# Optimization experiments

Hardware: AMD Instinct MI355X
Metric: run time of the kernel (lower is better)

Reference implementation:

```python
import jax, jax.numpy as jnp
import numpy as np
import math

HIDDEN = 1024

def setup_inputs() -> dict:
    key = jax.random.key(0)
    k1, k2, k3, k4, k5 = jax.random.split(key, 5)
    s = 1.0 / math.sqrt(HIDDEN)
    return {
        "x": jax.random.normal(k1, (4, 2048, HIDDEN), dtype=jnp.float32),
        "W_qkv": jax.random.uniform(k2, (HIDDEN, 3 * HIDDEN), jnp.float32, -s, s),
        "b_qkv": jax.random.uniform(k3, (3 * HIDDEN,), jnp.float32, -s, s),
        "W_out": jax.random.uniform(k4, (HIDDEN, HIDDEN), jnp.float32, -s, s),
        "b_out": jax.random.uniform(k5, (HIDDEN,), jnp.float32, -s, s),
    }

def reference(x, W_qkv, b_qkv, W_out, b_out):
    # fused QKV projection: [b, s, 3h]
    qkv = jnp.einsum("bsh,hd->bsd", x, W_qkv) + b_qkv
    q, k, v = jnp.split(qkv, 3, axis=-1)
    scale = 1.0 / math.sqrt(x.shape[-1])
    scores = jnp.einsum("bqh,bkh->bqk", q, k) * scale  # [b, s, s]
    attn = jax.nn.softmax(scores, axis=-1)
    out = jnp.einsum("bqk,bkh->bqh", attn, v)
    return jnp.einsum("bsh,hd->bsd", out, W_out) + b_out
```

## Files before the change

### kernel.cpp

```cpp
#include <hip/hip_runtime.h>
#include <cstdint>
#include <cstddef>


typedef __bf16 bf16;
typedef __bf16 bf16x8 __attribute__((ext_vector_type(8)));
typedef __bf16 bf16x4 __attribute__((ext_vector_type(4)));
typedef float  f32x4  __attribute__((ext_vector_type(4)));

#define THREADS 512
#define UNIT 8192

__device__ __forceinline__ void gload_lds16(const bf16* g, bf16* l) {
  __builtin_amdgcn_global_load_lds(
      (const __attribute__((address_space(1))) unsigned int*)g,
      (__attribute__((address_space(3))) unsigned int*)l, 16, 0, 0);
}

__device__ __forceinline__ void stage_unit(const bf16* g0, long ld, bf16* ldsu, int tid) {
  const int wv = tid >> 6;
  #pragma unroll
  for (int j = 0; j < 2; ++j) {
    const int c = j * 512 + tid;
    const int r = c >> 3;
    const int sg = (c & 7) ^ (r & 7);
    const int cb = j * 512 + (wv << 6);
    gload_lds16(g0 + (long)r * ld + sg * 8, ldsu + (size_t)cb * 8);
  }
}

__device__ __forceinline__ bf16x8 rd_frag(const bf16* unitb, int r, int s) {
  return *(const bf16x8*)(unitb + (size_t)r * 64 + (size_t)((s ^ (r & 7)) * 8));
}

#define GATE(N)  asm volatile("s_waitcnt vmcnt(" #N ")" ::: "memory")
#define LGKM0()  asm volatile("s_waitcnt lgkmcnt(0)" ::: "memory")
#define SBAR()   __builtin_amdgcn_s_barrier()
#define SCHED0() __builtin_amdgcn_sched_barrier(0)

#define BM2 256
#define BN2 128
#define BK2 64
#define BUFELS (3*UNIT)

template <int MODE>
__device__ __forceinline__ void gemm2_body(
    const bf16* __restrict__ A, long sAz, int lda,
    const bf16* __restrict__ B, long sBz, int ldb, int K,
    bf16* __restrict__ p0, long sCz, bf16* __restrict__ p1, bf16* __restrict__ p2,
    float* __restrict__ fout, const float* __restrict__ bias, float scale) {
  __shared__ bf16 lds[3 * BUFELS];
  const int tid = threadIdx.x;
  const int wv = tid >> 6, ln = tid & 63;
  const int wr = wv >> 1, wc = wv & 1;
  const int lr = ln & 15, lh = ln >> 4;
  const int m0 = blockIdx.x * BM2, n0 = blockIdx.y * BN2;
  const int z = blockIdx.z;
  A += (long)z * sAz;
  B += (long)z * sBz;
  const bf16* Ag = A + (long)m0 * lda;
  const bf16* Bg = B + (long)n0 * ldb;
  const int NT = K / BK2;

  #pragma unroll
  for (int t = 0; t < 2; ++t) {
    bf16* bb = lds + t * BUFELS;
    stage_unit(Ag + t * BK2, lda, bb, tid);
    stage_unit(Ag + (long)128 * lda + t * BK2, lda, bb + UNIT, tid);
    stage_unit(Bg + t * BK2, ldb, bb + 2 * UNIT, tid);
  }
  GATE(6);
  SCHED0();
  SBAR();

  f32x4 acc[4][4];
  #pragma unroll
  for (int i = 0; i < 4; ++i)
    #pragma unroll
    for (int j = 0; j < 4; ++j)
      acc[i][j] = f32x4{0.f, 0.f, 0.f, 0.f};

  const int aru = (wr & 1) * 64;
  const int au  = wr >> 1;

  int buf = 0, nb = 2;
  for (int t = 0; t < NT; ++t) {
    const bf16* Au = lds + buf * BUFELS + au * UNIT;
    const bf16* Bu = lds + buf * BUFELS + 2 * UNIT;
    bf16* Pn = lds + nb * BUFELS;
    const bool pf = (t + 2 < NT);
    bf16x8 aF[2][2], bF[4][2];

    #pragma unroll
    for (int i = 0; i < 2; ++i)
      #pragma unroll
      for (int ks = 0; ks < 2; ++ks)
        aF[i][ks] = rd_frag(Au, aru + i * 16 + lr, (ks << 2) + lh);
    #pragma unroll
    for (int nf = 0; nf < 4; ++nf)
      #pragma unroll
      for (int ks = 0; ks < 2; ++ks)
        bF[nf][ks] = rd_frag(Bu, wc * 64 + nf * 16 + lr, (ks << 2) + lh);
    if (pf) {
      stage_unit(Ag + (long)(t + 2) * BK2, lda, Pn, tid);
      stage_unit(Ag + (long)128 * lda + (long)(t + 2) * BK2, lda, Pn + UNIT, tid);
    }
    SBAR();
    LGKM0();
    SCHED0();
    __builtin_amdgcn_s_setprio(1);
    #pragma unroll
    for (int i = 0; i < 2; ++i)
      #pragma unroll
      for (int nf = 0; nf < 4; ++nf)
        #pragma unroll
        for (int ks = 0; ks < 2; ++ks)
          acc[i][nf] = __builtin_amdgcn_mfma_f32_16x16x32_bf16(aF[i][ks], bF[nf][ks], acc[i][nf], 0, 0, 0);
    __builtin_amdgcn_s_setprio(0);
    SBAR();

    #pragma unroll
    for (int i = 0; i < 2; ++i)
      #pragma unroll
      for (int ks = 0; ks < 2; ++ks)
        aF[i][ks] = rd_frag(Au, aru + 32 + i * 16 + lr, (ks << 2) + lh);
    if (pf) stage_unit(Bg + (long)(t + 2) * BK2, ldb, Pn + 2 * UNIT, tid);
    SBAR();
    LGKM0();
    SCHED0();
    __builtin_amdgcn_s_setprio(1);
    #pragma unroll
    for (int i = 0; i < 2; ++i)
      #pragma unroll
      for (int nf = 0; nf < 4; ++nf)
        #pragma unroll
        for (int ks = 0; ks < 2; ++ks)
          acc[2 + i][nf] = __builtin_amdgcn_mfma_f32_16x16x32_bf16(aF[i][ks], bF[nf][ks], acc[2 + i][nf], 0, 0, 0);
    __builtin_amdgcn_s_setprio(0);
    if (t + 1 < NT) {
      if (pf) { GATE(6); } else { GATE(0); }
      SCHED0();
    }
    SBAR();

    buf = (buf == 2) ? 0 : buf + 1;
    nb  = (nb == 2) ? 0 : nb + 1;
  }

  #pragma unroll
  for (int mf = 0; mf < 4; ++mf) {
    #pragma unroll
    for (int nf = 0; nf < 4; ++nf) {
      #pragma unroll
      for (int rg = 0; rg < 4; ++rg) {
        const int gm = m0 + wr * 64 + mf * 16 + lh * 4 + rg;
        const int gn = n0 + wc * 64 + nf * 16 + lr;
        float v = acc[mf][nf][rg];
        if constexpr (MODE == 0) {
          v += bias[gn];
          if (gn < 1024)       p0[(size_t)gm * 1024 + gn] = (bf16)v;
          else if (gn < 2048)  p1[(size_t)gm * 1024 + (gn - 1024)] = (bf16)v;
          else                 p2[(size_t)gm * 1024 + (gn - 2048)] = (bf16)v;
        } else if constexpr (MODE == 2) {
          p0[(size_t)z * sCz + (size_t)gm * 1024 + gn] = (bf16)v;
        } else {
          fout[(size_t)gm * 1024 + gn] = v + bias[gn];
        }
      }
    }
  }
}

#define GEMM_ARGS const bf16* A, long sAz, int lda, const bf16* B, long sBz, int ldb, \
                  int K, bf16* p0, long sCz, bf16* p1, bf16* p2, float* fout,         \
                  const float* bias, float scale
__global__ __launch_bounds__(THREADS, 2) void gemm_qkv(GEMM_ARGS) {
  gemm2_body<0>(A, sAz, lda, B, sBz, ldb, K, p0, sCz, p1, p2, fout, bias, scale);
}
__global__ __launch_bounds__(THREADS, 2) void gemm_pv(GEMM_ARGS) {
  gemm2_body<2>(A, sAz, lda, B, sBz, ldb, K, p0, sCz, p1, p2, fout, bias, scale);
}
__global__ __launch_bounds__(THREADS, 2) void gemm_out(GEMM_ARGS) {
  gemm2_body<3>(A, sAz, lda, B, sBz, ldb, K, p0, sCz, p1, p2, fout, bias, scale);
}

#define BM8 256
#define BN8 256

#define PHASE(DB, MH, NH, RA, RB, STAGE_CODE, GATE_CODE)                         \
  {                                                                              \
    if (RA) {                                                                    \
      _Pragma("unroll") for (int mf = 0; mf < 4; ++mf)                           \
        _Pragma("unroll") for (int ks = 0; ks < 2; ++ks)                         \
          aF[mf][ks] = rd_frag(&lds[DB][MH][0], wsm * 64 + mf * 16 + lr, ks * 4 + lh); \
    }                                                                            \
    if (RB) {                                                                    \
      _Pragma("unroll") for (int nf = 0; nf < 2; ++nf)                           \
        _Pragma("unroll") for (int ks = 0; ks < 2; ++ks)                         \
          bF[NH][nf][ks] = rd_frag(&lds[DB][2 + NH][0], wsn * 32 + nf * 16 + lr, ks * 4 + lh); \
    }                                                                            \
    STAGE_CODE;                                                                  \
    SBAR();                                                                      \
    LGKM0();                                                                     \
    SCHED0();                                                                    \
    __builtin_amdgcn_s_setprio(1);                                               \
    _Pragma("unroll") for (int mf = 0; mf < 4; ++mf)                             \
      _Pragma("unroll") for (int nf = 0; nf < 2; ++nf)                           \
        _Pragma("unroll") for (int ks = 0; ks < 2; ++ks)                         \
          acc[(MH)*4 + mf][(NH)*2 + nf] = __builtin_amdgcn_mfma_f32_16x16x32_bf16( \
              aF[mf][ks], bF[NH][nf][ks], acc[(MH)*4 + mf][(NH)*2 + nf], 0, 0, 0); \
    __builtin_amdgcn_s_setprio(0);                                               \
    GATE_CODE;                                                                   \
    SBAR();                                                                      \
    SCHED0();                                                                    \
  }

__global__ __launch_bounds__(THREADS, 2) void gemm_sc(
    const bf16* __restrict__ A, long sAz, int lda,
    const bf16* __restrict__ B, long sBz, int ldb, int K,
    bf16* __restrict__ p0, long sCz, float scale) {
  __shared__ bf16 lds[2][4][UNIT];
  const int tid = threadIdx.x;
  const int wv = tid >> 6, ln = tid & 63;
  const int wsm = wv >> 2, wsn = wv & 3;
  const int lr = ln & 15, lh = ln >> 4;

  const int gx = gridDim.x, gy = gridDim.y;
  const int lin = blockIdx.x + gx * (blockIdx.y + gy * blockIdx.z);
  const int nwg = gx * gy * gridDim.z;
  const int swz = (lin & 7) * (nwg >> 3) + (lin >> 3);
  const int by = swz % gy;
  const int t2 = swz / gy;
  const int bx = t2 % gx;
  const int z  = t2 / gx;

  const int m0 = bx * BM8, n0 = by * BN8;
  const bf16* Ag = A + (long)z * sAz + (long)m0 * lda;
  const bf16* Bg = B + (long)z * sBz + (long)n0 * ldb;
  const int NITER = K / 128;

  stage_unit(Ag,             lda, &lds[0][0][0], tid);
  stage_unit(Bg,             ldb, &lds[0][2][0], tid);
  stage_unit(Ag + 128 * lda, lda, &lds[0][1][0], tid);
  stage_unit(Bg + 128 * ldb, ldb, &lds[0][3][0], tid);
  stage_unit(Ag + 64,        lda, &lds[1][0][0], tid);
  stage_unit(Bg + 64,        ldb, &lds[1][2][0], tid);
  GATE(8);
  SBAR();
  SCHED0();

  f32x4 acc[8][4];
  #pragma unroll
  for (int i = 0; i < 8; ++i)
    #pragma unroll
    for (int j = 0; j < 4; ++j) acc[i][j] = f32x4{0.f, 0.f, 0.f, 0.f};
  bf16x8 aF[4][2], bF[2][2][2];

  for (int it = 0; it < NITER; ++it) {
    const bool nl = (it + 1 < NITER);
    const long ktA = 2L * it + 1, ktB = 2L * it + 2, ktC = 2L * it + 3;
    PHASE(0, 0, 0, 1, 1,
      { stage_unit(Ag + 128 * lda + ktA * 64, lda, &lds[1][1][0], tid); },
      { GATE(6); });
    PHASE(0, 0, 1, 0, 1,
      { stage_unit(Bg + 128 * ldb + ktA * 64, ldb, &lds[1][3][0], tid); },
      { GATE(10); });
    PHASE(0, 1, 0, 1, 0,
      { if (nl) stage_unit(Ag + ktB * 64, lda, &lds[0][0][0], tid); },
      {});
    PHASE(0, 1, 1, 0, 0,
      { if (nl) stage_unit(Bg + ktB * 64, ldb, &lds[0][2][0], tid); },
      { if (nl) { GATE(8); } else { GATE(4); } });
    PHASE(1, 0, 0, 1, 1,
      { if (nl) stage_unit(Ag + 128 * lda + ktB * 64, lda, &lds[0][1][0], tid); },
      { if (nl) { GATE(6); } else { GATE(0); } });
    PHASE(1, 0, 1, 0, 1,
      { if (nl) stage_unit(Bg + 128 * ldb + ktB * 64, ldb, &lds[0][3][0], tid); },
      { GATE(10); });
    PHASE(1, 1, 0, 1, 0,
      { if (nl) stage_unit(Ag + ktC * 64, lda, &lds[1][0][0], tid); },
      {});
    PHASE(1, 1, 1, 0, 0,
      { if (nl) stage_unit(Bg + ktC * 64, ldb, &lds[1][2][0], tid); },
      { GATE(8); });
  }

  #pragma unroll
  for (int mi = 0; mi < 8; ++mi) {
    #pragma unroll
    for (int ni = 0; ni < 4; ++ni) {
      #pragma unroll
      for (int rg = 0; rg < 4; ++rg) {
        const int gm = m0 + (mi >> 2) * 128 + wsm * 64 + (mi & 3) * 16 + lh * 4 + rg;
        const int gn = n0 + (ni >> 1) * 128 + wsn * 32 + (ni & 1) * 16 + lr;
        p0[(size_t)z * sCz + (size_t)gm * 2048 + gn] = (bf16)(acc[mi][ni][rg] * scale);
      }
    }
  }
}

__global__ __launch_bounds__(256) void k_f32_to_bf16(const float* __restrict__ in,
                                                     bf16* __restrict__ out, long n) {
  long i = ((long)blockIdx.x * blockDim.x + threadIdx.x) * 4;
  if (i + 3 < n) {
    float4 v = *(const float4*)(in + i);
    bf16x4 o;
    o[0] = (bf16)v.x; o[1] = (bf16)v.y; o[2] = (bf16)v.z; o[3] = (bf16)v.w;
    *(bf16x4*)(out + i) = o;
  }
}

__global__ __launch_bounds__(256) void k_transpose(const float* __restrict__ in,
                                                   bf16* __restrict__ out, int R, int C) {
  __shared__ float t[32][33];
  int c0 = blockIdx.x * 32, r0 = blockIdx.y * 32;
  int tx = threadIdx.x, ty = threadIdx.y;
  #pragma unroll
  for (int dy = 0; dy < 32; dy += 8)
    t[ty + dy][tx] = in[(size_t)(r0 + ty + dy) * C + c0 + tx];
  __syncthreads();
  #pragma unroll
  for (int dy = 0; dy < 32; dy += 8)
    out[(size_t)(c0 + ty + dy) * R + r0 + tx] = (bf16)t[tx][ty + dy];
}

__global__ __launch_bounds__(256) void k_transpose_v(const bf16* __restrict__ in,
                                                     bf16* __restrict__ out) {
  __shared__ bf16 t[64][65];
  const int z = blockIdx.z;
  in  += (size_t)z * 2048 * 1024;
  out += (size_t)z * 1024 * 2048;
  int h0 = blockIdx.x * 64, s0 = blockIdx.y * 64;
  int tx = threadIdx.x, ty = threadIdx.y;
  #pragma unroll
  for (int dy = 0; dy < 64; dy += 4)
    t[ty + dy][tx] = in[(size_t)(s0 + ty + dy) * 1024 + h0 + tx];
  __syncthreads();
  #pragma unroll
  for (int dy = 0; dy < 64; dy += 4)
    out[(size_t)(h0 + ty + dy) * 2048 + s0 + tx] = t[tx][ty + dy];
}

__global__ __launch_bounds__(256) void k_softmax(bf16* __restrict__ S) {
  const int row = blockIdx.x;
  bf16* p = S + (size_t)row * 2048;
  const int tid = threadIdx.x;
  bf16x8 vin = *(const bf16x8*)(p + tid * 8);
  float x[8];
  float mx = -1e30f;
  #pragma unroll
  for (int i = 0; i < 8; ++i) { x[i] = (float)vin[i]; mx = fmaxf(mx, x[i]); }
  #pragma unroll
  for (int off = 32; off; off >>= 1) mx = fmaxf(mx, __shfl_down(mx, off));
  __shared__ float redm[4];
  if ((tid & 63) == 0) redm[tid >> 6] = mx;
  __syncthreads();
  mx = fmaxf(fmaxf(redm[0], redm[1]), fmaxf(redm[2], redm[3]));
  float s = 0.f;
  #pragma unroll
  for (int i = 0; i < 8; ++i) { x[i] = __expf(x[i] - mx); s += x[i]; }
  #pragma unroll
  for (int off = 32; off; off >>= 1) s += __shfl_down(s, off);
  __shared__ float reds[4];
  if ((tid & 63) == 0) reds[tid >> 6] = s;
  __syncthreads();
  s = reds[0] + reds[1] + reds[2] + reds[3];
  float inv = 1.0f / s;
  bf16x8 vo;
  #pragma unroll
  for (int i = 0; i < 8; ++i) vo[i] = (bf16)(x[i] * inv);
  *(bf16x8*)(p + tid * 8) = vo;
}

extern "C" void kernel_launch(void* const* d_in, const int* in_sizes, int n_in,
                              void* d_out, int out_size, void* d_ws, size_t ws_size,
                              hipStream_t stream) {
  const float* x    = (const float*)d_in[0];
  const float* Wqkv = (const float*)d_in[1];
  const float* bqkv = (const float*)d_in[2];
  const float* Wout = (const float*)d_in[3];
  const float* bout = (const float*)d_in[4];
  float* out = (float*)d_out;

  char* w = (char*)d_ws;
  const size_t MB = 1ull << 20;
  bf16* Xb  = (bf16*)(w);
  bf16* WqT = (bf16*)(w + 16 * MB);
  bf16* WoT = (bf16*)(w + 22 * MB);
  bf16* Qb  = (bf16*)(w + 24 * MB);
  bf16* Kb  = (bf16*)(w + 40 * MB);
  bf16* Vb  = (bf16*)(w + 56 * MB);
  bf16* Sb  = (bf16*)(w + 72 * MB);
  bf16* AO  = (bf16*)(w + 104 * MB);
  bf16* VT  = Xb;

  k_f32_to_bf16<<<8192, 256, 0, stream>>>(x, Xb, 8388608L);
  dim3 tb(32, 8);
  k_transpose<<<dim3(96, 32), tb, 0, stream>>>(Wqkv, WqT, 1024, 3072);
  k_transpose<<<dim3(32, 32), tb, 0, stream>>>(Wout, WoT, 1024, 1024);

  gemm_qkv<<<dim3(32, 24), THREADS, 0, stream>>>(
      Xb, 0L, 1024, WqT, 0L, 1024, 1024, Qb, 0L, Kb, Vb, nullptr, bqkv, 1.0f);

  k_transpose_v<<<dim3(16, 32, 4), dim3(64, 4), 0, stream>>>(Vb, VT);

  gemm_sc<<<dim3(8, 8, 4), THREADS, 0, stream>>>(
      Qb, 2048L * 1024, 1024, Kb, 2048L * 1024, 1024, 1024,
      Sb, 2048L * 2048, 0.03125f);

  k_softmax<<<8192, 256, 0, stream>>>(Sb);

  gemm_pv<<<dim3(8, 8, 4), THREADS, 0, stream>>>(
      Sb, 2048L * 2048, 2048, VT, 1024L * 2048, 2048, 2048,
      AO, 2048L * 1024, nullptr, nullptr, nullptr, nullptr, 1.0f);

  gemm_out<<<dim3(32, 8), THREADS, 0, stream>>>(
      AO, 0L, 1024, WoT, 0L, 1024, 1024,
      nullptr, 0L, nullptr, nullptr, out, bout, 1.0f);
}
```

Baseline: 217.4 us.

## Replace 256x128 GEMM tiles with 128x128 BK32 tiles for QKV, PV, and out projections

The QKV, PV and output-projection GEMMs move from a 512-thread 256x128 tile with BK=64 to a 256-thread 128x128 tile with BK=32 and a triple-buffered LDS ring. The LDS swizzle changes to suit 32-wide rows, and the K loop is simplified to one fragment load and one MFMA phase per step. The aim is more workgroups and higher occupancy (launch bounds 256,3), which should fill the CUs better on these grid sizes. In exchange, each tile reuses loaded data less and needs more barriers per unit of K work.

New measurement: 212.8 us. 1.02x faster.

```diff
diff --git a/kernel.cpp b/kernel.cpp
--- a/kernel.cpp
+++ b/kernel.cpp
@@ -8,7 +8,6 @@
 typedef __bf16 bf16x4 __attribute__((ext_vector_type(4)));
 typedef float  f32x4  __attribute__((ext_vector_type(4)));
 
-#define THREADS 512
 #define UNIT 8192
 
 __device__ __forceinline__ void gload_lds16(const bf16* g, bf16* l) {
@@ -17,59 +16,52 @@
       (__attribute__((address_space(3))) unsigned int*)l, 16, 0, 0);
 }
 
-__device__ __forceinline__ void stage_unit(const bf16* g0, long ld, bf16* ldsu, int tid) {
-  const int wv = tid >> 6;
-  #pragma unroll
-  for (int j = 0; j < 2; ++j) {
-    const int c = j * 512 + tid;
-    const int r = c >> 3;
-    const int sg = (c & 7) ^ (r & 7);
-    const int cb = j * 512 + (wv << 6);
-    gload_lds16(g0 + (long)r * ld + sg * 8, ldsu + (size_t)cb * 8);
-  }
-}
-
-__device__ __forceinline__ bf16x8 rd_frag(const bf16* unitb, int r, int s) {
-  return *(const bf16x8*)(unitb + (size_t)r * 64 + (size_t)((s ^ (r & 7)) * 8));
-}
-
 #define GATE(N)  asm volatile("s_waitcnt vmcnt(" #N ")" ::: "memory")
 #define LGKM0()  asm volatile("s_waitcnt lgkmcnt(0)" ::: "memory")
 #define SBAR()   __builtin_amdgcn_s_barrier()
 #define SCHED0() __builtin_amdgcn_sched_barrier(0)
 
-#define BM2 256
-#define BN2 128
-#define BK2 64
-#define BUFELS (3*UNIT)
+#define BK97 32
+#define U97  4096
+
+__device__ __forceinline__ void stage97(const bf16* g0, long ld, bf16* u, int tid) {
+  const int wv = tid >> 6;
+  #pragma unroll
+  for (int j = 0; j < 2; ++j) {
+    const int c = j * 256 + tid;
+    const int r = c >> 2, s = c & 3;
+    const int sg = s ^ ((r >> 1) & 3);
+    const int cb = j * 256 + (wv << 6);
+    gload_lds16(g0 + (long)r * ld + sg * 8, u + (size_t)cb * 8);
+  }
+}
+
+__device__ __forceinline__ bf16x8 rd97(const bf16* u, int r, int s) {
+  return *(const bf16x8*)(u + (size_t)r * 32 + (size_t)((s ^ ((r >> 1) & 3)) * 8));
+}
 
 template <int MODE>
-__device__ __forceinline__ void gemm2_body(
+__device__ __forceinline__ void gemm97_body(
     const bf16* __restrict__ A, long sAz, int lda,
     const bf16* __restrict__ B, long sBz, int ldb, int K,
     bf16* __restrict__ p0, long sCz, bf16* __restrict__ p1, bf16* __restrict__ p2,
     float* __restrict__ fout, const float* __restrict__ bias, float scale) {
-  __shared__ bf16 lds[3 * BUFELS];
+  __shared__ bf16 lds[3][2][U97];
   const int tid = threadIdx.x;
   const int wv = tid >> 6, ln = tid & 63;
   const int wr = wv >> 1, wc = wv & 1;
   const int lr = ln & 15, lh = ln >> 4;
-  const int m0 = blockIdx.x * BM2, n0 = blockIdx.y * BN2;
+  const int m0 = blockIdx.x * 128, n0 = blockIdx.y * 128;
   const int z = blockIdx.z;
-  A += (long)z * sAz;
-  B += (long)z * sBz;
-  const bf16* Ag = A + (long)m0 * lda;
-  const bf16* Bg = B + (long)n0 * ldb;
-  const int NT = K / BK2;
-
-  #pragma unroll
-  for (int t = 0; t < 2; ++t) {
-    bf16* bb = lds + t * BUFELS;
-    stage_unit(Ag + t * BK2, lda, bb, tid);
-    stage_unit(Ag + (long)128 * lda + t * BK2, lda, bb + UNIT, tid);
-    stage_unit(Bg + t * BK2, ldb, bb + 2 * UNIT, tid);
-  }
-  GATE(6);
+  const bf16* Ag = A + (long)z * sAz + (long)m0 * lda;
+  const bf16* Bg = B + (long)z * sBz + (long)n0 * ldb;
+  const int NT = K / BK97;
+
+  stage97(Ag,        lda, &lds[0][0][0], tid);
+  stage97(Bg,        ldb, &lds[0][1][0], tid);
+  stage97(Ag + BK97, lda, &lds[1][0][0], tid);
+  stage97(Bg + BK97, ldb, &lds[1][1][0], tid);
+  GATE(4);
   SCHED0();
   SBAR();
 
@@ -77,74 +69,38 @@
   #pragma unroll
   for (int i = 0; i < 4; ++i)
     #pragma unroll
-    for (int j = 0; j < 4; ++j)
-      acc[i][j] = f32x4{0.f, 0.f, 0.f, 0.f};
-
-  const int aru = (wr & 1) * 64;
-  const int au  = wr >> 1;
-
-  int buf = 0, nb = 2;
+    for (int j = 0; j < 4; ++j) acc[i][j] = f32x4{0.f, 0.f, 0.f, 0.f};
+
+  int rs = 0, ns = 2;
   for (int t = 0; t < NT; ++t) {
-    const bf16* Au = lds + buf * BUFELS + au * UNIT;
-    const bf16* Bu = lds + buf * BUFELS + 2 * UNIT;
-    bf16* Pn = lds + nb * BUFELS;
+    const bf16* Au = &lds[rs][0][0];
+    const bf16* Bu = &lds[rs][1][0];
     const bool pf = (t + 2 < NT);
-    bf16x8 aF[2][2], bF[4][2];
-
-    #pragma unroll
-    for (int i = 0; i < 2; ++i)
-      #pragma unroll
-      for (int ks = 0; ks < 2; ++ks)
-        aF[i][ks] = rd_frag(Au, aru + i * 16 + lr, (ks << 2) + lh);
-    #pragma unroll
-    for (int nf = 0; nf < 4; ++nf)
-      #pragma unroll
-      for (int ks = 0; ks < 2; ++ks)
-        bF[nf][ks] = rd_frag(Bu, wc * 64 + nf * 16 + lr, (ks << 2) + lh);
+    bf16x8 aF[4], bF[4];
+    #pragma unroll
+    for (int i = 0; i < 4; ++i) aF[i] = rd97(Au, wr * 64 + i * 16 + lr, lh);
+    #pragma unroll
+    for (int j = 0; j < 4; ++j) bF[j] = rd97(Bu, wc * 64 + j * 16 + lr, lh);
     if (pf) {
-      stage_unit(Ag + (long)(t + 2) * BK2, lda, Pn, tid);
-      stage_unit(Ag + (long)128 * lda + (long)(t + 2) * BK2, lda, Pn + UNIT, tid);
+      stage97(Ag + (long)(t + 2) * BK97, lda, &lds[ns][0][0], tid);
+      stage97(Bg + (long)(t + 2) * BK97, ldb, &lds[ns][1][0], tid);
     }
-    SBAR();
     LGKM0();
     SCHED0();
     __builtin_amdgcn_s_setprio(1);
     #pragma unroll
-    for (int i = 0; i < 2; ++i)
+    for (int i = 0; i < 4; ++i)
       #pragma unroll
-      for (int nf = 0; nf < 4; ++nf)
-        #pragma unroll
-        for (int ks = 0; ks < 2; ++ks)
-          acc[i][nf] = __builtin_amdgcn_mfma_f32_16x16x32_bf16(aF[i][ks], bF[nf][ks], acc[i][nf], 0, 0, 0);
-    __builtin_amdgcn_s_setprio(0);
-    SBAR();
-
-    #pragma unroll
-    for (int i = 0; i < 2; ++i)
-      #pragma unroll
-      for (int ks = 0; ks < 2; ++ks)
-        aF[i][ks] = rd_frag(Au, aru + 32 + i * 16 + lr, (ks << 2) + lh);
-    if (pf) stage_unit(Bg + (long)(t + 2) * BK2, ldb, Pn + 2 * UNIT, tid);
-    SBAR();
-    LGKM0();
-    SCHED0();
-    __builtin_amdgcn_s_setprio(1);
-    #pragma unroll
-    for (int i = 0; i < 2; ++i)
-      #pragma unroll
-      for (int nf = 0; nf < 4; ++nf)
-        #pragma unroll
-        for (int ks = 0; ks < 2; ++ks)
-          acc[2 + i][nf] = __builtin_amdgcn_mfma_f32_16x16x32_bf16(aF[i][ks], bF[nf][ks], acc[2 + i][nf], 0, 0, 0);
+      for (int j = 0; j < 4; ++j)
+        acc[i][j] = __builtin_amdgcn_mfma_f32_16x16x32_bf16(aF[i], bF[j], acc[i][j], 0, 0, 0);
     __builtin_amdgcn_s_setprio(0);
     if (t + 1 < NT) {
-      if (pf) { GATE(6); } else { GATE(0); }
+      if (pf) { GATE(4); } else { GATE(0); }
       SCHED0();
+      SBAR();
     }
-    SBAR();
-
-    buf = (buf == 2) ? 0 : buf + 1;
-    nb  = (nb == 2) ? 0 : nb + 1;
+    rs = (rs == 2) ? 0 : rs + 1;
+    ns = (ns == 2) ? 0 : ns + 1;
   }
 
   #pragma unroll
@@ -174,18 +130,33 @@
 #define GEMM_ARGS const bf16* A, long sAz, int lda, const bf16* B, long sBz, int ldb, \
                   int K, bf16* p0, long sCz, bf16* p1, bf16* p2, float* fout,         \
                   const float* bias, float scale
-__global__ __launch_bounds__(THREADS, 2) void gemm_qkv(GEMM_ARGS) {
-  gemm2_body<0>(A, sAz, lda, B, sBz, ldb, K, p0, sCz, p1, p2, fout, bias, scale);
-}
-__global__ __launch_bounds__(THREADS, 2) void gemm_pv(GEMM_ARGS) {
-  gemm2_body<2>(A, sAz, lda, B, sBz, ldb, K, p0, sCz, p1, p2, fout, bias, scale);
-}
-__global__ __launch_bounds__(THREADS, 2) void gemm_out(GEMM_ARGS) {
-  gemm2_body<3>(A, sAz, lda, B, sBz, ldb, K, p0, sCz, p1, p2, fout, bias, scale);
-}
-
-#define BM8 256
-#define BN8 256
+__global__ __launch_bounds__(256, 3) void gemm_qkv(GEMM_ARGS) {
+  gemm97_body<0>(A, sAz, lda, B, sBz, ldb, K, p0, sCz, p1, p2, fout, bias, scale);
+}
+__global__ __launch_bounds__(256, 3) void gemm_pv(GEMM_ARGS) {
+  gemm97_body<2>(A, sAz, lda, B, sBz, ldb, K, p0, sCz, p1, p2, fout, bias, scale);
+}
+__global__ __launch_bounds__(256, 3) void gemm_out(GEMM_ARGS) {
+  gemm97_body<3>(A, sAz, lda, B, sBz, ldb, K, p0, sCz, p1, p2, fout, bias, scale);
+}
+
+#define THREADS8 512
+
+__device__ __forceinline__ void stage_unit(const bf16* g0, long ld, bf16* ldsu, int tid) {
+  const int wv = tid >> 6;
+  #pragma unroll
+  for (int j = 0; j < 2; ++j) {
+    const int c = j * 512 + tid;
+    const int r = c >> 3;
+    const int sg = (c & 7) ^ (r & 7);
+    const int cb = j * 512 + (wv << 6);
+    gload_lds16(g0 + (long)r * ld + sg * 8, ldsu + (size_t)cb * 8);
+  }
+}
+
+__device__ __forceinline__ bf16x8 rd_frag(const bf16* unitb, int r, int s) {
+  return *(const bf16x8*)(unitb + (size_t)r * 64 + (size_t)((s ^ (r & 7)) * 8));
+}
 
 #define PHASE(DB, MH, NH, RA, RB, STAGE_CODE, GATE_CODE)                         \
   {                                                                              \
@@ -215,7 +186,7 @@
     SCHED0();                                                                    \
   }
 
-__global__ __launch_bounds__(THREADS, 2) void gemm_sc(
+__global__ __launch_bounds__(THREADS8, 2) void gemm_sc(
     const bf16* __restrict__ A, long sAz, int lda,
     const bf16* __restrict__ B, long sBz, int ldb, int K,
     bf16* __restrict__ p0, long sCz, float scale) {
@@ -234,7 +205,7 @@
   const int bx = t2 % gx;
   const int z  = t2 / gx;
 
-  const int m0 = bx * BM8, n0 = by * BN8;
+  const int m0 = bx * 256, n0 = by * 256;
   const bf16* Ag = A + (long)z * sAz + (long)m0 * lda;
   const bf16* Bg = B + (long)z * sBz + (long)n0 * ldb;
   const int NITER = K / 128;
@@ -399,22 +370,22 @@
   k_transpose<<<dim3(96, 32), tb, 0, stream>>>(Wqkv, WqT, 1024, 3072);
   k_transpose<<<dim3(32, 32), tb, 0, stream>>>(Wout, WoT, 1024, 1024);
 
-  gemm_qkv<<<dim3(32, 24), THREADS, 0, stream>>>(
+  gemm_qkv<<<dim3(64, 24), 256, 0, stream>>>(
       Xb, 0L, 1024, WqT, 0L, 1024, 1024, Qb, 0L, Kb, Vb, nullptr, bqkv, 1.0f);
 
   k_transpose_v<<<dim3(16, 32, 4), dim3(64, 4), 0, stream>>>(Vb, VT);
 
-  gemm_sc<<<dim3(8, 8, 4), THREADS, 0, stream>>>(
+  gemm_sc<<<dim3(8, 8, 4), THREADS8, 0, stream>>>(
       Qb, 2048L * 1024, 1024, Kb, 2048L * 1024, 1024, 1024,
       Sb, 2048L * 2048, 0.03125f);
 
   k_softmax<<<8192, 256, 0, stream>>>(Sb);
 
-  gemm_pv<<<dim3(8, 8, 4), THREADS, 0, stream>>>(
+  gemm_pv<<<dim3(16, 8, 4), 256, 0, stream>>>(
       Sb, 2048L * 2048, 2048, VT, 1024L * 2048, 2048, 2048,
       AO, 2048L * 1024, nullptr, nullptr, nullptr, nullptr, 1.0f);
 
-  gemm_out<<<dim3(32, 8), THREADS, 0, stream>>>(
+  gemm_out<<<dim3(64, 8), 256, 0, stream>>>(
       AO, 0L, 1024, WoT, 0L, 1024, 1024,
       nullptr, 0L, nullptr, nullptr, out, bout, 1.0f);
 }
```
